# Performance work log

Hardware: AMD Instinct MI355X
Metric: run time of the kernel (lower is better)

The kernel has to match this reference:

```python
import jax, jax.numpy as jnp
import numpy as np

B, T, D, H, E = 32, 512, 768, 12, 6  # batch, seq(=input_size), n_embd, num_heads, per-head dim
DFF = 4 * D
EPS = 1e-5


def setup_inputs() -> dict:
    key = jax.random.key(0)
    ks = jax.random.split(key, 10)
    s = 0.02
    return {
        "x": jax.random.normal(ks[0], (B, T, D), jnp.float32),
        "Wq": jax.random.normal(ks[1], (H, D, E), jnp.float32) * s,
        "Wk": jax.random.normal(ks[2], (H, D, E), jnp.float32) * s,
        "Wv": jax.random.normal(ks[3], (H, D, E), jnp.float32) * s,
        "Wo": jax.random.normal(ks[4], (H * E, D), jnp.float32) * s,
        "bo": jnp.zeros((D,), jnp.float32),
        "W1": jax.random.normal(ks[5], (D, DFF), jnp.float32) * s,
        "b1": jnp.zeros((DFF,), jnp.float32),
        "W2": jax.random.normal(ks[6], (DFF, D), jnp.float32) * s,
        "b2": jnp.zeros((D,), jnp.float32),
        "g1": jnp.ones((D,), jnp.float32),
        "beta1": jnp.zeros((D,), jnp.float32),
        "g2": jnp.ones((D,), jnp.float32),
        "beta2": jnp.zeros((D,), jnp.float32),
    }


def _layernorm(x, g, b):
    m = jnp.mean(x, axis=-1, keepdims=True)
    v = jnp.var(x, axis=-1, keepdims=True)  # biased, matches torch LayerNorm
    return (x - m) * jax.lax.rsqrt(v + EPS) * g + b


def reference(x, Wq, Wk, Wv, Wo, bo, W1, b1, W2, b2, g1, beta1, g2, beta2):
    # --- pre-LN multi-head causal attention (dropout = identity, eval mode) ---
    xn = _layernorm(x, g1, beta1)
    q = jnp.einsum("btd,hde->bhte", xn, Wq)
    k = jnp.einsum("btd,hde->bhte", xn, Wk)
    v = jnp.einsum("btd,hde->bhte", xn, Wv)
    scores = jnp.einsum("bhte,bhse->bhts", q, k) * (E ** -0.5)
    causal = jnp.tril(jnp.ones((T, T), dtype=bool))
    scores = jnp.where(causal, scores, -jnp.inf)
    w = jax.nn.softmax(scores, axis=-1)
    o = jnp.einsum("bhts,bhse->bhte", w, v)
    o = o.transpose(0, 2, 1, 3).reshape(B, T, H * E)  # concat heads -> [B,T,72]
    x = x + o @ Wo + bo
    # --- pre-LN feed-forward ---
    y = _layernorm(x, g2, beta2)
    ff = jax.nn.relu(y @ W1 + b1) @ W2 + b2
    return x + ff
```

## Files before the change

### kernel.cpp

```cpp
#include <hip/hip_runtime.h>
#include <hip/hip_bf16.h>

#define BT 16384
#define DIM 768
#define NH 12
#define DFF 3072

typedef __attribute__((ext_vector_type(8))) short short8;
typedef __attribute__((ext_vector_type(4))) float floatx4;
typedef __attribute__((ext_vector_type(4))) unsigned short ushort4b;

using bf16 = __hip_bfloat16;

static __device__ __forceinline__ float b2f(bf16 v) { return __bfloat162float(v); }
static __device__ __forceinline__ bf16 f2b(float v) { return __float2bfloat16(v); }

static __device__ __forceinline__ void gload_lds16(const void* g, void* l) {
    __builtin_amdgcn_global_load_lds(
        (const __attribute__((address_space(1))) unsigned int*)g,
        (__attribute__((address_space(3))) unsigned int*)l, 16, 0, 0);
}

__global__ __launch_bounds__(256) void pack_small_kernel(
    const float* __restrict__ Wq, const float* __restrict__ Wk, const float* __restrict__ Wv,
    const float* __restrict__ Wo, bf16* __restrict__ wqkv, bf16* __restrict__ wo_t)
{
    int i = blockIdx.x * 256 + threadIdx.x;
    const int S0 = 256 * 768, S1 = 768 * 96;
    if (i < S0) {
        int c = i / 768, dd = i % 768;
        float v = 0.f;
        if (c < 216) {
            int sel = c / 72, cc = c % 72, h = cc / 6, e = cc % 6;
            const float* W = (sel == 0) ? Wq : (sel == 1) ? Wk : Wv;
            v = W[((size_t)h * 768 + dd) * 6 + e];
        }
        wqkv[i] = f2b(v);
    } else if ((i -= S0) < S1) {
        int n = i / 96, r = i % 96;
        wo_t[i] = f2b(r < 72 ? Wo[r * 768 + n] : 0.f);
    }
}

__global__ __launch_bounds__(256) void transpose_kernel(
    const float* __restrict__ in, bf16* __restrict__ out, int R, int C)
{
    __shared__ float t[32][33];
    int c0 = blockIdx.x * 32, r0 = blockIdx.y * 32;
    int cx = threadIdx.x & 31, ry = threadIdx.x >> 5;
#pragma unroll
    for (int j = 0; j < 4; j++)
        t[ry + j * 8][cx] = in[(size_t)(r0 + ry + j * 8) * C + c0 + cx];
    __syncthreads();
    int rx = cx, cy = ry;
#pragma unroll
    for (int j = 0; j < 4; j++)
        out[(size_t)(c0 + cy + j * 8) * R + r0 + rx] = f2b(t[rx][cy + j * 8]);
}

__global__ __launch_bounds__(192) void ln_kernel(
    const float* __restrict__ x, const float* __restrict__ g, const float* __restrict__ be,
    bf16* __restrict__ out)
{
    int row = blockIdx.x;
    int tid = threadIdx.x;
    const float4* xr = (const float4*)(x + (size_t)row * DIM);
    float4 v = xr[tid];
    float s = v.x + v.y + v.z + v.w;
    float s2 = v.x * v.x + v.y * v.y + v.z * v.z + v.w * v.w;
#pragma unroll
    for (int off = 32; off; off >>= 1) {
        s += __shfl_down(s, off);
        s2 += __shfl_down(s2, off);
    }
    __shared__ float red[6];
    int wv = tid >> 6, ln = tid & 63;
    if (ln == 0) { red[wv] = s; red[3 + wv] = s2; }
    __syncthreads();
    float ts = red[0] + red[1] + red[2];
    float ts2 = red[3] + red[4] + red[5];
    float mean = ts * (1.f / 768.f);
    float var = ts2 * (1.f / 768.f) - mean * mean;
    float rstd = rsqrtf(var + 1e-5f);
    int c = tid * 4;
    float o0 = (v.x - mean) * rstd * g[c + 0] + be[c + 0];
    float o1 = (v.y - mean) * rstd * g[c + 1] + be[c + 1];
    float o2 = (v.z - mean) * rstd * g[c + 2] + be[c + 2];
    float o3 = (v.w - mean) * rstd * g[c + 3] + be[c + 3];
    bf16 h0 = f2b(o0), h1 = f2b(o1), h2 = f2b(o2), h3 = f2b(o3);
    ushort4b pk;
    pk[0] = *(unsigned short*)&h0; pk[1] = *(unsigned short*)&h1;
    pk[2] = *(unsigned short*)&h2; pk[3] = *(unsigned short*)&h3;
    *(ushort4b*)(out + (size_t)row * DIM + c) = pk;
}

template <int NSLAB, bool RELU, bool BIAS, bool RES, bool BF16OUT>
__global__ __launch_bounds__(256) void gemm_kernel(
    const bf16* __restrict__ A, const bf16* __restrict__ Bt,
    const float* __restrict__ bias, const float* __restrict__ res,
    void* __restrict__ Cv, int M, int N, int K)
{
    constexpr int SMEM_BYTES = BF16OUT ? (128 * 136 * 2) : (NSLAB * 2 * 128 * 32 * 2);
    __shared__ __align__(16) char smem[SMEM_BYTES];
    bf16* lA = (bf16*)smem;
    bf16* lB = lA + NSLAB * 128 * 32;

    const int tid = threadIdx.x;
    const int bm = blockIdx.x * 128;
    const int bn = blockIdx.y * 128;
    const int wave = tid >> 6, lane = tid & 63;
    const int wm = (wave >> 1) * 64, wn = (wave & 1) * 64;
    const int quad = lane >> 4, l16 = lane & 15;
    const int lrow = lane >> 2;
    const int lkc = (lane & 3) * 8;

    floatx4 acc[4][4] = {};

    for (int k0 = 0; k0 < K; k0 += NSLAB * 32) {
#pragma unroll
        for (int s = 0; s < NSLAB; s++) {
#pragma unroll
            for (int it = 0; it < 2; it++) {
                int r = wave * 32 + it * 16;
                gload_lds16(A + (size_t)(bm + r + lrow) * K + k0 + s * 32 + lkc,
                            lA + s * 4096 + r * 32);
                gload_lds16(Bt + (size_t)(bn + r + lrow) * K + k0 + s * 32 + lkc,
                            lB + s * 4096 + r * 32);
            }
        }
        __syncthreads();
#pragma unroll
        for (int s = 0; s < NSLAB; s++) {
            short8 af[4], bfr[4];
#pragma unroll
            for (int mt = 0; mt < 4; mt++)
                af[mt] = *(const short8*)(lA + s * 4096 + (wm + mt * 16 + l16) * 32 + quad * 8);
#pragma unroll
            for (int nt = 0; nt < 4; nt++)
                bfr[nt] = *(const short8*)(lB + s * 4096 + (wn + nt * 16 + l16) * 32 + quad * 8);
#pragma unroll
            for (int mt = 0; mt < 4; mt++)
#pragma unroll
                for (int nt = 0; nt < 4; nt++)
                    acc[mt][nt] = __builtin_amdgcn_mfma_f32_16x16x32_bf16(af[mt], bfr[nt], acc[mt][nt], 0, 0, 0);
        }
        __syncthreads();
    }

    if constexpr (BF16OUT) {
        bf16* ltile = (bf16*)smem;
#pragma unroll
        for (int mt = 0; mt < 4; mt++) {
#pragma unroll
            for (int nt = 0; nt < 4; nt++) {
                int tc = wn + nt * 16 + l16;
#pragma unroll
                for (int r = 0; r < 4; r++) {
                    int tr = wm + mt * 16 + quad * 4 + r;
                    float v0 = acc[mt][nt][r];
                    if constexpr (BIAS) v0 += bias[bn + tc];
                    if constexpr (RELU) v0 = fmaxf(v0, 0.f);
                    ltile[tr * 136 + tc] = f2b(v0);
                }
            }
        }
        __syncthreads();
        bf16* C = (bf16*)Cv;
        int rr0 = tid >> 4, col8 = (tid & 15) * 8;
        int gc = bn + col8;
#pragma unroll
        for (int p = 0; p < 8; p++) {
            int rr = p * 16 + rr0;
            if (gc < N)
                *(short8*)(C + (size_t)(bm + rr) * N + gc) =
                    *(const short8*)(ltile + rr * 136 + col8);
        }
    } else {
        float* C = (float*)Cv;
#pragma unroll
        for (int mt = 0; mt < 4; mt++) {
#pragma unroll
            for (int nt = 0; nt < 4; nt++) {
                int gc = bn + wn + nt * 16 + l16;
                if (gc < N) {
#pragma unroll
                    for (int r = 0; r < 4; r++) {
                        int gr = bm + wm + mt * 16 + quad * 4 + r;
                        float v0 = acc[mt][nt][r];
                        if constexpr (BIAS) v0 += bias[gc];
                        if constexpr (RES) v0 += res[(size_t)gr * N + gc];
                        if constexpr (RELU) v0 = fmaxf(v0, 0.f);
                        C[(size_t)gr * N + gc] = v0;
                    }
                }
            }
        }
    }
}

template <bool RELU, bool BIAS, bool RES, bool BF16OUT>
__global__ __launch_bounds__(512, 2) void gemm192_kernel(
    const bf16* __restrict__ A, const bf16* __restrict__ Bt,
    const float* __restrict__ bias, const float* __restrict__ res,
    void* __restrict__ Cv, int M, int N, int K)
{
    extern __shared__ __align__(16) char smem[];
    const int NT = K >> 6;
    const int nbm = M >> 8;
    const int nwg = nbm * (N / 192);
    int idx = blockIdx.x;
    idx = (idx & 7) * (nwg >> 3) + (idx >> 3);
    const int bm = (idx % nbm) << 8;
    const int bn = (idx / nbm) * 192;

    const int tid = threadIdx.x;
    const int w = tid >> 6, lane = tid & 63;
    const int wm = w >> 1, wn = w & 1;
    const int l16 = lane & 15, quad = lane >> 4;

    const int rstg = (w >> 1) * 16 + (lane >> 2);
    const int cstg = (w & 1) * 32 + (((lane & 3) * 8) ^ ((lane & 32) ? 16 : 0));
    const bf16* aSrc = A + (size_t)(bm + rstg) * K + cstg;
    const bf16* bSrc = Bt + (size_t)(bn + rstg) * K + cstg;
    const int stgoff = w * 1024;

    const int xr = (quad * 16) ^ ((l16 & 8) ? 32 : 0);
    const int aoff = wm * 8192 + l16 * 64 + xr;
    const int boff = 32768 + wn * 12288 + l16 * 64 + xr;

#define STG(BO, ISB, CH, T) gload_lds16( \
        ((ISB) ? bSrc : aSrc) + (size_t)(CH) * 64 * K + (size_t)(T) * 64, \
        smem + (BO) + (ISB) * 32768 + (CH) * 8192 + stgoff)

#define BARX() asm volatile("s_barrier" ::: "memory")
#define VMW(N_) asm volatile("s_waitcnt vmcnt(" #N_ ")" ::: "memory")

    floatx4 acc[4][6] = {};
    short8 a[2][2][2], b[2][3][2];

#define LDA(QM, CB) { _Pragma("unroll") for (int fm = 0; fm < 2; fm++) { \
    _Pragma("unroll") for (int s = 0; s < 2; s++) \
        a[QM][fm][s] = *(const short8*)((CB) + aoff + (QM) * 4096 + fm * 2048 + s * 1024); } }
#define LDB(QN, CB) { _Pragma("unroll") for (int fn = 0; fn < 3; fn++) { \
    _Pragma("unroll") for (int s = 0; s < 2; s++) \
        b[QN][fn][s] = *(const short8*)((CB) + boff + (QN) * 6144 + fn * 2048 + s * 1024); } }
#define MM(QM, QN) { __builtin_amdgcn_s_setprio(1); \
    _Pragma("unroll") for (int fm = 0; fm < 2; fm++) { \
    _Pragma("unroll") for (int fn = 0; fn < 3; fn++) { \
    _Pragma("unroll") for (int s = 0; s < 2; s++) \
        acc[(QM)*2+fm][(QN)*3+fn] = __builtin_amdgcn_mfma_f32_16x16x32_bf16( \
            a[QM][fm][s], b[(QN)][fn][s], acc[(QM)*2+fm][(QN)*3+fn], 0, 0, 0); } } \
    __builtin_amdgcn_s_setprio(0); }

#pragma unroll
    for (int c = 0; c < 4; c++) STG(0, 0, c, 0);
#pragma unroll
    for (int c = 0; c < 3; c++) STG(0, 1, c, 0);
#pragma unroll
    for (int c = 0; c < 4; c++) STG(57344, 0, c, 1);
#pragma unroll
    for (int c = 0; c < 3; c++) STG(57344, 1, c, 1);
    VMW(7);
    BARX();
    LDA(0, smem); LDB(0, smem);

    for (int g = 0; g < NT; ++g) {
        const int bo = (g & 1) * 57344;
        const char* cb = smem + bo;
        const char* nb = smem + (bo ^ 57344);
        LDA(1, cb);
        MM(0, 0);
        BARX();
        LDB(1, cb);
        MM(1, 0);
        BARX();
        if (g + 2 < NT) { STG(bo, 0, 0, g + 2); STG(bo, 0, 1, g + 2);
                          STG(bo, 0, 2, g + 2); STG(bo, 0, 3, g + 2); }
        MM(1, 1);
        if (g + 2 < NT) { VMW(4); } else { VMW(0); }
        BARX();
        if (g + 1 < NT) LDB(0, nb);
        if (g + 2 < NT) { STG(bo, 1, 0, g + 2); STG(bo, 1, 1, g + 2); STG(bo, 1, 2, g + 2); }
        MM(0, 1);
        if (g + 1 < NT) LDA(0, nb);
        BARX();
    }

    if constexpr (BF16OUT) {
        bf16* lt = (bf16*)smem;
#pragma unroll
        for (int mf = 0; mf < 4; mf++) {
            const int row = wm * 64 + mf * 16 + quad * 4;
#pragma unroll
            for (int nf = 0; nf < 6; nf++) {
                const int col = wn * 96 + nf * 16 + l16;
                float bv = BIAS ? bias[bn + col] : 0.f;
#pragma unroll
                for (int r = 0; r < 4; r++) {
                    float v = acc[mf][nf][r] + bv;
                    if constexpr (RELU) v = fmaxf(v, 0.f);
                    lt[(row + r) * 200 + col] = f2b(v);
                }
            }
        }
        __syncthreads();
        bf16* C = (bf16*)Cv;
#pragma unroll
        for (int it = 0; it < 12; it++) {
            int c = it * 512 + tid;
            int rr = c / 24, cc = (c - rr * 24) * 8;
            *(short8*)(C + (size_t)(bm + rr) * N + bn + cc) =
                *(const short8*)(lt + rr * 200 + cc);
        }
    } else {
        float* C = (float*)Cv;
#pragma unroll
        for (int mf = 0; mf < 4; mf++) {
            const int gr = bm + wm * 64 + mf * 16 + quad * 4;
#pragma unroll
            for (int nf = 0; nf < 6; nf++) {
                const int gc = bn + wn * 96 + nf * 16 + l16;
                float bv = BIAS ? bias[gc] : 0.f;
#pragma unroll
                for (int r = 0; r < 4; r++) {
                    float v = acc[mf][nf][r] + bv;
                    if constexpr (RES) v += res[(size_t)(gr + r) * N + gc];
                    if constexpr (RELU) v = fmaxf(v, 0.f);
                    C[(size_t)(gr + r) * N + gc] = v;
                }
            }
        }
    }
#undef STG
#undef BARX
#undef VMW
#undef LDA
#undef LDB
#undef MM
}

__global__ __launch_bounds__(256) void attn_kernel(const bf16* __restrict__ qkv, bf16* __restrict__ o_pad)
{
    int blk = blockIdx.x;
    int half = blk & 1;
    int bh = blk >> 1;
    int b = bh / NH, h = bh % NH;
    int wave = threadIdx.x >> 6, lane = threadIdx.x & 63;
    const int jmap0[4] = {0, 2, 5, 7}, jmap1[4] = {1, 3, 4, 6};
    int j = half ? jmap1[wave] : jmap0[wave];
    int t = j * 64 + lane;
    int smax = half ? 448 : 512;

    __shared__ float ks[512 * 6];
    __shared__ float vs[512 * 6];
    const bf16* base = qkv + (size_t)b * 512 * 216;
    for (int i = threadIdx.x; i < smax * 6; i += 256) {
        int s = i / 6, e = i % 6;
        ks[i] = b2f(base[s * 216 + 72 + h * 6 + e]);
        vs[i] = b2f(base[s * 216 + 144 + h * 6 + e]);
    }
    __syncthreads();

    float q0 = b2f(base[t * 216 + h * 6 + 0]);
    float q1 = b2f(base[t * 216 + h * 6 + 1]);
    float q2 = b2f(base[t * 216 + h * 6 + 2]);
    float q3 = b2f(base[t * 216 + h * 6 + 3]);
    float q4 = b2f(base[t * 216 + h * 6 + 4]);
    float q5 = b2f(base[t * 216 + h * 6 + 5]);

    const float scale = 0.4082482904638630f;
    float m = -1e30f, l = 0.f;
    float o0 = 0, o1 = 0, o2 = 0, o3 = 0, o4 = 0, o5 = 0;
    for (int s = 0; s <= t; s++) {
        const float* kk = &ks[s * 6];
        float sc = (q0 * kk[0] + q1 * kk[1] + q2 * kk[2] + q3 * kk[3] + q4 * kk[4] + q5 * kk[5]) * scale;
        float nm = fmaxf(m, sc);
        float alpha = __expf(m - nm);
        float p = __expf(sc - nm);
        l = l * alpha + p;
        const float* vv = &vs[s * 6];
        o0 = o0 * alpha + p * vv[0];
        o1 = o1 * alpha + p * vv[1];
        o2 = o2 * alpha + p * vv[2];
        o3 = o3 * alpha + p * vv[3];
        o4 = o4 * alpha + p * vv[4];
        o5 = o5 * alpha + p * vv[5];
        m = nm;
    }
    float inv = 1.f / l;
    bf16* orow = o_pad + (size_t)(b * 512 + t) * 96 + h * 6;
    orow[0] = f2b(o0 * inv);
    orow[1] = f2b(o1 * inv);
    orow[2] = f2b(o2 * inv);
    orow[3] = f2b(o3 * inv);
    orow[4] = f2b(o4 * inv);
    orow[5] = f2b(o5 * inv);
}

extern "C" void kernel_launch(void* const* d_in, const int* in_sizes, int n_in,
                              void* d_out, int out_size, void* d_ws, size_t ws_size,
                              hipStream_t stream)
{
    const float* x   = (const float*)d_in[0];
    const float* Wq  = (const float*)d_in[1];
    const float* Wk  = (const float*)d_in[2];
    const float* Wv  = (const float*)d_in[3];
    const float* Wo  = (const float*)d_in[4];
    const float* bo  = (const float*)d_in[5];
    const float* W1  = (const float*)d_in[6];
    const float* b1  = (const float*)d_in[7];
    const float* W2  = (const float*)d_in[8];
    const float* b2  = (const float*)d_in[9];
    const float* g1  = (const float*)d_in[10];
    const float* be1 = (const float*)d_in[11];
    const float* g2  = (const float*)d_in[12];
    const float* be2 = (const float*)d_in[13];

    char* ws = (char*)d_ws;
    size_t off = 0;
    auto alloc = [&](size_t bytes) {
        void* p = ws + off;
        off = (off + bytes + 255) & ~(size_t)255;
        return p;
    };
    bf16*  xn    = (bf16*)alloc((size_t)BT * DIM * 2);
    bf16*  qkvb  = (bf16*)alloc((size_t)BT * 216 * 2);
    bf16*  o_pad = (bf16*)alloc((size_t)BT * 96 * 2);
    float* x1    = (float*)alloc((size_t)BT * DIM * 4);
    bf16*  ffb   = (bf16*)alloc((size_t)BT * DFF * 2);
    bf16*  wqkv  = (bf16*)alloc((size_t)256 * 768 * 2);
    bf16*  wo_t  = (bf16*)alloc((size_t)768 * 96 * 2);
    bf16*  w1t   = (bf16*)alloc((size_t)3072 * 768 * 2);
    bf16*  w2t   = (bf16*)alloc((size_t)768 * 3072 * 2);

    hipFuncSetAttribute(reinterpret_cast<const void*>(&gemm192_kernel<true, true, false, true>),
                        hipFuncAttributeMaxDynamicSharedMemorySize, 114688);
    hipFuncSetAttribute(reinterpret_cast<const void*>(&gemm192_kernel<false, true, true, false>),
                        hipFuncAttributeMaxDynamicSharedMemorySize, 114688);

    const int PACK_N = 256 * 768 + 768 * 96;
    pack_small_kernel<<<(PACK_N + 255) / 256, 256, 0, stream>>>(Wq, Wk, Wv, Wo, wqkv, wo_t);
    transpose_kernel<<<dim3(3072 / 32, 768 / 32), 256, 0, stream>>>(W1, w1t, 768, 3072);
    transpose_kernel<<<dim3(768 / 32, 3072 / 32), 256, 0, stream>>>(W2, w2t, 3072, 768);

    ln_kernel<<<BT, 192, 0, stream>>>(x, g1, be1, xn);
    gemm_kernel<2, false, false, false, true><<<dim3(128, 2), 256, 0, stream>>>(
        xn, wqkv, nullptr, nullptr, qkvb, BT, 216, 768);
    attn_kernel<<<32 * NH * 2, 256, 0, stream>>>(qkvb, o_pad);
    gemm_kernel<1, false, true, true, false><<<dim3(128, 6), 256, 0, stream>>>(
        o_pad, wo_t, bo, x, x1, BT, 768, 96);
    ln_kernel<<<BT, 192, 0, stream>>>(x1, g2, be2, xn);
    gemm192_kernel<true, true, false, true><<<1024, 512, 114688, stream>>>(
        xn, w1t, b1, nullptr, ffb, BT, 3072, 768);
    gemm192_kernel<false, true, true, false><<<256, 512, 114688, stream>>>(
        ffb, w2t, b2, x1, (float*)d_out, BT, 768, 3072);
}
```

Baseline: 437.5 us.

## Make FFN1 GEMM persistent over four N-tiles per workgroup, pipelining across tiles

```diff
diff --git a/kernel.cpp b/kernel.cpp
--- a/kernel.cpp
+++ b/kernel.cpp
@@ -198,20 +198,19 @@
     }
 }
 
-template <bool RELU, bool BIAS, bool RES, bool BF16OUT>
+template <int NTC, int TPB, bool RELU, bool BIAS, bool RES, bool BF16OUT>
 __global__ __launch_bounds__(512, 2) void gemm192_kernel(
     const bf16* __restrict__ A, const bf16* __restrict__ Bt,
     const float* __restrict__ bias, const float* __restrict__ res,
-    void* __restrict__ Cv, int M, int N, int K)
-{
+    void* __restrict__ Cv, int N)
+{
+    constexpr int KC = NTC * 64;
+    constexpr int NG = NTC * TPB;
     extern __shared__ __align__(16) char smem[];
-    const int NT = K >> 6;
-    const int nbm = M >> 8;
-    const int nwg = nbm * (N / 192);
-    int idx = blockIdx.x;
-    idx = (idx & 7) * (nwg >> 3) + (idx >> 3);
-    const int bm = (idx % nbm) << 8;
-    const int bn = (idx / nbm) * 192;
+
+    const int sid = ((blockIdx.x & 7) << 5) + (blockIdx.x >> 3);
+    const int bm = (sid & 63) << 8;
+    const int bnBase = (sid >> 6) * (TPB * 192);
 
     const int tid = threadIdx.x;
     const int w = tid >> 6, lane = tid & 63;
@@ -220,20 +219,21 @@
 
     const int rstg = (w >> 1) * 16 + (lane >> 2);
     const int cstg = (w & 1) * 32 + (((lane & 3) * 8) ^ ((lane & 32) ? 16 : 0));
-    const bf16* aSrc = A + (size_t)(bm + rstg) * K + cstg;
-    const bf16* bSrc = Bt + (size_t)(bn + rstg) * K + cstg;
+    const bf16* aSrc = A + (size_t)(bm + rstg) * KC + cstg;
+    const bf16* bSrc = Bt + (size_t)(bnBase + rstg) * KC + cstg;
     const int stgoff = w * 1024;
 
     const int xr = (quad * 16) ^ ((l16 & 8) ? 32 : 0);
     const int aoff = wm * 8192 + l16 * 64 + xr;
     const int boff = 32768 + wn * 12288 + l16 * 64 + xr;
 
-#define STG(BO, ISB, CH, T) gload_lds16( \
-        ((ISB) ? bSrc : aSrc) + (size_t)(CH) * 64 * K + (size_t)(T) * 64, \
+#define STG2(BO, ISB, CH) gload_lds16( \
+        ((ISB) ? bS2 : aS2) + (size_t)(CH) * 64 * KC, \
         smem + (BO) + (ISB) * 32768 + (CH) * 8192 + stgoff)
 
 #define BARX() asm volatile("s_barrier" ::: "memory")
 #define VMW(N_) asm volatile("s_waitcnt vmcnt(" #N_ ")" ::: "memory")
+#define LGW0() asm volatile("s_waitcnt lgkmcnt(0)" ::: "memory")
 
     floatx4 acc[4][6] = {};
     short8 a[2][2][2], b[2][3][2];
@@ -252,68 +252,99 @@
             a[QM][fm][s], b[(QN)][fn][s], acc[(QM)*2+fm][(QN)*3+fn], 0, 0, 0); } } \
     __builtin_amdgcn_s_setprio(0); }
 
-#pragma unroll
-    for (int c = 0; c < 4; c++) STG(0, 0, c, 0);
-#pragma unroll
-    for (int c = 0; c < 3; c++) STG(0, 1, c, 0);
-#pragma unroll
-    for (int c = 0; c < 4; c++) STG(57344, 0, c, 1);
-#pragma unroll
-    for (int c = 0; c < 3; c++) STG(57344, 1, c, 1);
+    {
+        const bf16* aS2 = aSrc;           const bf16* bS2 = bSrc;
+#pragma unroll
+        for (int c = 0; c < 4; c++) STG2(0, 0, c);
+#pragma unroll
+        for (int c = 0; c < 3; c++) STG2(0, 1, c);
+        aS2 = aSrc + 64; bS2 = bSrc + 64;
+#pragma unroll
+        for (int c = 0; c < 4; c++) STG2(57344, 0, c);
+#pragma unroll
+        for (int c = 0; c < 3; c++) STG2(57344, 1, c);
+    }
     VMW(7);
     BARX();
     LDA(0, smem); LDB(0, smem);
 
-    for (int g = 0; g < NT; ++g) {
-        const int bo = (g & 1) * 57344;
+    for (int G = 0; G < NG; ++G) {
+        const int bo = (G & 1) * 57344;
         const char* cb = smem + bo;
         const char* nb = smem + (bo ^ 57344);
+        const int v = G + 2;
+        const bf16* aS2 = aSrc;
+        const bf16* bS2 = bSrc;
+        if (v < NG) {
+            const int t2 = v / NTC, g2 = v - t2 * NTC;
+            aS2 = aSrc + (size_t)g2 * 64;
+            bS2 = bSrc + (size_t)t2 * (192 * (size_t)KC) + (size_t)g2 * 64;
+        }
         LDA(1, cb);
         MM(0, 0);
         BARX();
         LDB(1, cb);
         MM(1, 0);
         BARX();
-        if (g + 2 < NT) { STG(bo, 0, 0, g + 2); STG(bo, 0, 1, g + 2);
-                          STG(bo, 0, 2, g + 2); STG(bo, 0, 3, g + 2); }
+        if (v < NG) { STG2(bo, 0, 0); STG2(bo, 0, 1); STG2(bo, 0, 2); STG2(bo, 0, 3); }
         MM(1, 1);
-        if (g + 2 < NT) { VMW(4); } else { VMW(0); }
+        if (G < NG - 2) { VMW(4); } else { VMW(0); }
         BARX();
-        if (g + 1 < NT) LDB(0, nb);
-        if (g + 2 < NT) { STG(bo, 1, 0, g + 2); STG(bo, 1, 1, g + 2); STG(bo, 1, 2, g + 2); }
+        if (G + 1 < NG) LDB(0, nb);
+        if (v < NG) { STG2(bo, 1, 0); STG2(bo, 1, 1); STG2(bo, 1, 2); }
         MM(0, 1);
-        if (g + 1 < NT) LDA(0, nb);
+        if (G + 1 < NG) LDA(0, nb);
         BARX();
-    }
-
-    if constexpr (BF16OUT) {
-        bf16* lt = (bf16*)smem;
-#pragma unroll
-        for (int mf = 0; mf < 4; mf++) {
-            const int row = wm * 64 + mf * 16 + quad * 4;
-#pragma unroll
-            for (int nf = 0; nf < 6; nf++) {
-                const int col = wn * 96 + nf * 16 + l16;
-                float bv = BIAS ? bias[bn + col] : 0.f;
-#pragma unroll
-                for (int r = 0; r < 4; r++) {
-                    float v = acc[mf][nf][r] + bv;
-                    if constexpr (RELU) v = fmaxf(v, 0.f);
-                    lt[(row + r) * 200 + col] = f2b(v);
+
+        if constexpr (BF16OUT) {
+            if ((G % NTC) == NTC - 1) {
+                const int t = G / NTC;
+                const int bnt = bnBase + t * 192;
+                bf16* sc = (bf16*)(smem + 114688);
+                bf16* C = (bf16*)Cv;
+#pragma unroll
+                for (int ci = 0; ci < 4; ci++) {
+                    if (wn == (ci >> 1)) {
+                        const int nfh = ci & 1;
+#pragma unroll
+                        for (int mf = 0; mf < 4; mf++) {
+#pragma unroll
+                            for (int n3 = 0; n3 < 3; n3++) {
+                                const int nf = nfh * 3 + n3;
+                                const int row = wm * 64 + mf * 16 + quad * 4;
+                                float bv = BIAS ? bias[bnt + wn * 96 + nf * 16 + l16] : 0.f;
+#pragma unroll
+                                for (int r = 0; r < 4; r++) {
+                                    float vv = acc[mf][nf][r] + bv;
+                                    if constexpr (RELU) vv = fmaxf(vv, 0.f);
+                                    sc[(row + r) * 56 + n3 * 16 + l16] = f2b(vv);
+                                }
+                            }
+                        }
+                    }
+                    LGW0();
+                    BARX();
+#pragma unroll
+                    for (int it = 0; it < 3; it++) {
+                        int c = it * 512 + tid;
+                        int rr = c / 6, cc = (c - rr * 6) * 8;
+                        *(short8*)(C + (size_t)(bm + rr) * N + bnt + ci * 48 + cc) =
+                            *(const short8*)(sc + rr * 56 + cc);
+                    }
+                    BARX();
                 }
+#pragma unroll
+                for (int mf = 0; mf < 4; mf++)
+#pragma unroll
+                    for (int nf = 0; nf < 6; nf++)
+                        acc[mf][nf] = (floatx4){0.f, 0.f, 0.f, 0.f};
             }
         }
-        __syncthreads();
-        bf16* C = (bf16*)Cv;
-#pragma unroll
-        for (int it = 0; it < 12; it++) {
-            int c = it * 512 + tid;
-            int rr = c / 24, cc = (c - rr * 24) * 8;
-            *(short8*)(C + (size_t)(bm + rr) * N + bn + cc) =
-                *(const short8*)(lt + rr * 200 + cc);
-        }
-    } else {
+    }
+
+    if constexpr (!BF16OUT) {
         float* C = (float*)Cv;
+        const int bn = bnBase;
 #pragma unroll
         for (int mf = 0; mf < 4; mf++) {
             const int gr = bm + wm * 64 + mf * 16 + quad * 4;
@@ -331,9 +362,10 @@
             }
         }
     }
-#undef STG
+#undef STG2
 #undef BARX
 #undef VMW
+#undef LGW0
 #undef LDA
 #undef LDB
 #undef MM
@@ -433,9 +465,9 @@
     bf16*  w1t   = (bf16*)alloc((size_t)3072 * 768 * 2);
     bf16*  w2t   = (bf16*)alloc((size_t)768 * 3072 * 2);
 
-    hipFuncSetAttribute(reinterpret_cast<const void*>(&gemm192_kernel<true, true, false, true>),
-                        hipFuncAttributeMaxDynamicSharedMemorySize, 114688);
-    hipFuncSetAttribute(reinterpret_cast<const void*>(&gemm192_kernel<false, true, true, false>),
+    hipFuncSetAttribute(reinterpret_cast<const void*>(&gemm192_kernel<12, 4, true, true, false, true>),
+                        hipFuncAttributeMaxDynamicSharedMemorySize, 143360);
+    hipFuncSetAttribute(reinterpret_cast<const void*>(&gemm192_kernel<48, 1, false, true, true, false>),
                         hipFuncAttributeMaxDynamicSharedMemorySize, 114688);
 
     const int PACK_N = 256 * 768 + 768 * 96;
@@ -450,8 +482,8 @@
     gemm_kernel<1, false, true, true, false><<<dim3(128, 6), 256, 0, stream>>>(
         o_pad, wo_t, bo, x, x1, BT, 768, 96);
     ln_kernel<<<BT, 192, 0, stream>>>(x1, g2, be2, xn);
-    gemm192_kernel<true, true, false, true><<<1024, 512, 114688, stream>>>(
-        xn, w1t, b1, nullptr, ffb, BT, 3072, 768);
-    gemm192_kernel<false, true, true, false><<<256, 512, 114688, stream>>>(
-        ffb, w2t, b2, x1, (float*)d_out, BT, 768, 3072);
-}
+    gemm192_kernel<12, 4, true, true, false, true><<<256, 512, 143360, stream>>>(
+        xn, w1t, b1, nullptr, ffb, 3072);
+    gemm192_kernel<48, 1, false, true, true, false><<<256, 512, 114688, stream>>>(
+        ffb, w2t, b2, x1, (float*)d_out, 768);
+}
```

New measurement: 439.0 us. No clear change (+0.3%).
